# Performance work log

Measured on AMD Instinct MI355X. Metric: run time of the kernel, lower is better.

Reference implementation:

```python
import jax, jax.numpy as jnp
import numpy as np


def setup_inputs() -> dict:
    key = jax.random.key(0)
    x = jax.random.normal(key, (128, 256, 32, 32), dtype=jnp.float32)
    return {"x": x, "iter_num": 5}


def reference(x, iter_num):
    # x: (B, C, H, W)
    B, C, H, W = x.shape
    N = H * W
    xr = x.reshape(B, C, N)
    # Covariance pooling: X @ I_hat @ X^T == (1/N) * Xc @ Xc^T  (I_hat = I/N - J/N^2)
    xc = xr - xr.mean(axis=2, keepdims=True)
    cov = jnp.einsum('bcn,bdn->bcd', xc, xc) / N  # (B, C, C)

    # Newton-Schulz iterative matrix square root
    I = jnp.eye(C, dtype=x.dtype)
    I3 = 3.0 * I
    trace = jnp.trace(cov, axis1=1, axis2=2)[:, None, None]  # norm_A = tr(cov)
    A = cov / trace
    ZY = 0.5 * (I3 - A)
    Y = A @ ZY
    Z = ZY
    for _ in range(1, iter_num - 1):
        ZY = 0.5 * (I3 - Z @ Y)
        Y = Y @ ZY
        Z = ZY @ Z
    YZY = 0.5 * (Y @ (I3 - Z @ Y))
    sqrtm = YZY * jnp.sqrt(trace)  # (B, C, C)

    # Upper-triangular vectorization (row-major, including diagonal)
    r, c = np.triu_indices(C)
    idx = jnp.asarray(r * C + c)
    return sqrtm.reshape(B, C * C)[:, idx]  # (B, C*(C+1)//2)
```

## Files before the change

### kernel.cpp

```cpp
#include <hip/hip_runtime.h>
#include <hip/hip_fp16.h>


typedef _Float16 half8 __attribute__((ext_vector_type(8)));
typedef _Float16 half4 __attribute__((ext_vector_type(4)));
typedef float f32x4 __attribute__((ext_vector_type(4)));

#define OUTPB 32896

__device__ __forceinline__ void gl_lds16(const void* g, void* l) {
  __builtin_amdgcn_global_load_lds(
      (const __attribute__((address_space(1))) void*)g,
      (__attribute__((address_space(3))) void*)l, 16, 0, 0);
}

#define VMB(N) asm volatile("s_waitcnt vmcnt(" #N ")\n\ts_barrier" ::: "memory")
#define LKB()  asm volatile("s_waitcnt lgkmcnt(0)\n\ts_barrier" ::: "memory")

__device__ __forceinline__ void tile_pq(int t, int& p, int& q) {
  p = (t > 3) + (t > 6) + (t > 8);
  int base = p * 4 - (p * (p - 1)) / 2;
  q = p + (t - base);
}

__device__ __forceinline__ half8 cvt8(float4 a, float4 b) {
  half8 h;
  h[0] = (_Float16)a.x; h[1] = (_Float16)a.y; h[2] = (_Float16)a.z; h[3] = (_Float16)a.w;
  h[4] = (_Float16)b.x; h[5] = (_Float16)b.y; h[6] = (_Float16)b.z; h[7] = (_Float16)b.w;
  return h;
}

__device__ __forceinline__ void mfma64(const _Float16* lA, const _Float16* lB,
                                       f32x4 (&acc)[2][2], int wr, int wc,
                                       int lr, int lk) {
#pragma unroll
  for (int ks = 0; ks < 2; ++ks) {
    half8 af[2], bf[2];
#pragma unroll
    for (int m = 0; m < 2; ++m) {
      int row = wr * 32 + m * 16 + lr;
      int kc = (ks * 4 + lk) ^ (row & 7);
      af[m] = *(const half8*)&lA[row * 64 + kc * 8];
    }
#pragma unroll
    for (int n = 0; n < 2; ++n) {
      int row = wc * 32 + n * 16 + lr;
      int kc = (ks * 4 + lk) ^ (row & 7);
      bf[n] = *(const half8*)&lB[row * 64 + kc * 8];
    }
    __builtin_amdgcn_s_setprio(1);
#pragma unroll
    for (int m = 0; m < 2; ++m)
#pragma unroll
      for (int n = 0; n < 2; ++n)
        acc[m][n] = __builtin_amdgcn_mfma_f32_16x16x32_f16(af[m], bf[n], acc[m][n], 0, 0, 0);
    __builtin_amdgcn_s_setprio(0);
  }
}

template <typename F>
__device__ __forceinline__ void store_sym(F f, _Float16* D, size_t boff, int p, int q,
    bool mirror, _Float16* ldsT, f32x4 (&acc)[2][2],
    int wr, int wc, int lr, int lk, int tid) {
#pragma unroll
  for (int m = 0; m < 2; ++m)
#pragma unroll
    for (int n = 0; n < 2; ++n) {
      int il0 = wr * 32 + m * 16 + lk * 4;
      int jl = wc * 32 + n * 16 + lr;
      half4 v4;
#pragma unroll
      for (int r = 0; r < 4; ++r) {
        _Float16 v = f(acc[m][n][r], p * 64 + il0 + r, q * 64 + jl);
        v4[r] = v;
        if (mirror) ldsT[(il0 + r) * 64 + (jl ^ (((il0 + r) & 7) << 3))] = v;
      }
      *(half4*)&D[boff + (size_t)(q * 64 + jl) * 256 + p * 64 + il0] = v4;
    }
  if (mirror) {
    __syncthreads();
#pragma unroll
    for (int pp = 0; pp < 2; ++pp) {
      int u = pp * 256 + tid;
      int im = u >> 3, cu = u & 7;
      half8 v8 = *(const half8*)&ldsT[im * 64 + ((cu ^ (im & 7)) << 3)];
      *(half8*)&D[boff + (size_t)(p * 64 + im) * 256 + q * 64 + cu * 8] = v8;
    }
  }
}

__global__ __launch_bounds__(256, 2) void k_cov(const float* __restrict__ x,
                                                _Float16* __restrict__ covh,
                                                float* __restrict__ trPart) {
  __shared__ float lds_f[16384];
  __shared__ float sred[4];

  const int lin = blockIdx.x + 10 * blockIdx.y;
  const int cid = (lin & 7) * 160 + (lin >> 3);
  const int b = cid / 10, t = cid - 10 * b;
  int p, q; tile_pq(t, p, q);
  const bool diag = (p == q);
  const int tid = threadIdx.x, w = tid >> 6, lane = tid & 63;
  const int wr = w >> 1, wc = w & 1, lr = lane & 15, lk = lane >> 4;

  const float* Ab = x + ((size_t)b * 256 + p * 64) * 1024;
  const float* Bb = x + ((size_t)b * 256 + q * 64) * 1024;

  f32x4 acc[2][2] = {};
  f32x4 rsA[2] = {}, rsB[2] = {};
  half8 ones;
#pragma unroll
  for (int i = 0; i < 8; ++i) ones[i] = (_Float16)1.0f;

  auto stageF = [&](const float* panel, int buf, int baseF, int kk) {
#pragma unroll
    for (int i = 0; i < 4; ++i) {
      int s = (w * 4 + i) * 64 + lane;
      int row = s >> 4, cst = s & 15;
      int kc = cst ^ (row & 15);
      gl_lds16(panel + (size_t)row * 1024 + kk * 64 + kc * 4,
               &lds_f[baseF + buf * 4096 + (w * 4 + i) * 256]);
    }
  };

  auto step = [&](const float* lA, const float* lB) {
#pragma unroll
    for (int ks = 0; ks < 2; ++ks) {
      half8 af[2], bf[2];
#pragma unroll
      for (int m = 0; m < 2; ++m) {
        int row = wr * 32 + m * 16 + lr;
        int msk = row & 15, c0 = ks * 8 + lk * 2;
        float4 f0 = *(const float4*)&lA[row * 64 + (c0 ^ msk) * 4];
        float4 f1 = *(const float4*)&lA[row * 64 + ((c0 + 1) ^ msk) * 4];
        af[m] = cvt8(f0, f1);
      }
#pragma unroll
      for (int n = 0; n < 2; ++n) {
        int row = wc * 32 + n * 16 + lr;
        int msk = row & 15, c0 = ks * 8 + lk * 2;
        float4 f0 = *(const float4*)&lB[row * 64 + (c0 ^ msk) * 4];
        float4 f1 = *(const float4*)&lB[row * 64 + ((c0 + 1) ^ msk) * 4];
        bf[n] = cvt8(f0, f1);
      }
      __builtin_amdgcn_s_setprio(1);
#pragma unroll
      for (int m = 0; m < 2; ++m)
        rsA[m] = __builtin_amdgcn_mfma_f32_16x16x32_f16(af[m], ones, rsA[m], 0, 0, 0);
#pragma unroll
      for (int n = 0; n < 2; ++n)
        rsB[n] = __builtin_amdgcn_mfma_f32_16x16x32_f16(ones, bf[n], rsB[n], 0, 0, 0);
#pragma unroll
      for (int m = 0; m < 2; ++m)
#pragma unroll
        for (int n = 0; n < 2; ++n)
          acc[m][n] = __builtin_amdgcn_mfma_f32_16x16x32_f16(af[m], bf[n], acc[m][n], 0, 0, 0);
      __builtin_amdgcn_s_setprio(0);
    }
  };

  stageF(Ab, 0, 0, 0);
  if (!diag) stageF(Bb, 0, 8192, 0);
#pragma unroll 1
  for (int kk = 0; kk < 16; ++kk) {
    int cur = kk & 1;
    if (kk < 15) {
      stageF(Ab, cur ^ 1, 0, kk + 1);
      if (!diag) stageF(Bb, cur ^ 1, 8192, kk + 1);
      if (diag) { VMB(4); } else { VMB(8); }
    } else {
      VMB(0);
    }
    step(&lds_f[cur * 4096], diag ? &lds_f[cur * 4096] : &lds_f[8192 + cur * 4096]);
    LKB();
  }

  const float inv = 1.f / 1024.f;
  if (diag) {
    float tp = 0.f;
#pragma unroll
    for (int m = 0; m < 2; ++m)
#pragma unroll
      for (int n = 0; n < 2; ++n)
#pragma unroll
        for (int r = 0; r < 4; ++r) {
          int il = wr * 32 + m * 16 + lk * 4 + r, jl = wc * 32 + n * 16 + lr;
          if (il == jl) tp += (acc[m][n][r] - rsA[m][r] * rsB[n][0] * inv) * inv;
        }
#pragma unroll
    for (int o = 32; o; o >>= 1) tp += __shfl_down(tp, o);
    if (lane == 0) sred[w] = tp;
    __syncthreads();
    if (tid == 0) trPart[b * 4 + p] = sred[0] + sred[1] + sred[2] + sred[3];
  }

  _Float16* ldsh = (_Float16*)lds_f;
  const size_t boff = (size_t)b * 65536;
#pragma unroll
  for (int m = 0; m < 2; ++m)
#pragma unroll
    for (int n = 0; n < 2; ++n) {
      int il0 = wr * 32 + m * 16 + lk * 4;
      int jl = wc * 32 + n * 16 + lr;
      half4 v4;
#pragma unroll
      for (int r = 0; r < 4; ++r) {
        float cv = (acc[m][n][r] - rsA[m][r] * rsB[n][0] * inv) * inv;
        v4[r] = (_Float16)cv;
        if (!diag) ldsh[(il0 + r) * 64 + (jl ^ (((il0 + r) & 7) << 3))] = v4[r];
      }
      *(half4*)&covh[boff + (size_t)(q * 64 + jl) * 256 + p * 64 + il0] = v4;
    }
  if (!diag) {
    __syncthreads();
#pragma unroll
    for (int pp = 0; pp < 2; ++pp) {
      int u = pp * 256 + tid;
      int im = u >> 3, cu = u & 7;
      half8 v8 = *(const half8*)&ldsh[im * 64 + ((cu ^ (im & 7)) << 3)];
      *(half8*)&covh[boff + (size_t)(p * 64 + im) * 256 + q * 64 + cu * 8] = v8;
    }
  }
}

enum { EPI_S2 = 0, EPI_ZY = 1, EPI_OUT = 2 };

struct GP {
  const _Float16 *A0, *B0;
  _Float16 *D0, *D1;
  const _Float16* covh;
  const float* trP;
  float* outF;
};

template <int EPI>
__global__ __launch_bounds__(256, 4) void k_gemm(GP g) {
  __shared__ _Float16 lds[(EPI == EPI_S2) ? 8192 : 16384];

  const int lin = blockIdx.x + 10 * blockIdx.y;
  const int cid = (lin & 7) * 160 + (lin >> 3);
  const int b = cid / 10, t = cid - 10 * b;
  int p, q; tile_pq(t, p, q);
  const bool diag = (p == q);
  constexpr bool share = (EPI == EPI_S2);
  const int tid = threadIdx.x, w = tid >> 6, lane = tid & 63;
  const int wr = w >> 1, wc = w & 1, lr = lane & 15, lk = lane >> 4;

  const size_t boff = (size_t)b * 65536;
  const _Float16* Ap = g.A0 + boff + (size_t)p * 64 * 256;
  const _Float16* Bp = (share ? g.A0 : g.B0) + boff + (size_t)q * 64 * 256;

  f32x4 acc[2][2] = {};

  auto stageH = [&](const _Float16* panel, int buf, int base, int kk) {
#pragma unroll
    for (int i = 0; i < 2; ++i) {
      int s = (w * 2 + i) * 64 + lane;
      int row = s >> 3, cst = s & 7;
      int kc = cst ^ (row & 7);
      gl_lds16(panel + (size_t)row * 256 + kk * 64 + kc * 8,
               &lds[base + buf * 4096 + (w * 2 + i) * 512]);
    }
  };

  stageH(Ap, 0, 0, 0);
  if (!share) stageH(Bp, 0, 8192, 0);
#pragma unroll 1
  for (int kk = 0; kk < 4; ++kk) {
    int cur = kk & 1;
    if (kk < 3) {
      stageH(Ap, cur ^ 1, 0, kk + 1);
      if (!share) stageH(Bp, cur ^ 1, 8192, kk + 1);
      if (share) { VMB(2); } else { VMB(4); }
    } else {
      VMB(0);
    }
    mfma64(&lds[cur * 4096], share ? &lds[cur * 4096] : &lds[8192 + cur * 4096],
           acc, wr, wc, lr, lk);
    LKB();
  }

  if constexpr (EPI == EPI_ZY) {
    store_sym([&](float a, int i, int j) {
                return (_Float16)((i == j ? 1.5f : 0.f) - 0.5f * a);
              }, g.D0, boff, p, q, !diag, lds, acc, wr, wc, lr, lk, tid);
  } else if constexpr (EPI == EPI_S2) {
    float tv = g.trP[b * 4] + g.trP[b * 4 + 1] + g.trP[b * 4 + 2] + g.trP[b * 4 + 3];
    float it1 = 1.f / tv;
    _Float16* TY = lds;
    _Float16* TZ = lds + 4096;
#pragma unroll
    for (int m = 0; m < 2; ++m)
#pragma unroll
      for (int n = 0; n < 2; ++n) {
        int il0 = wr * 32 + m * 16 + lk * 4;
        int jl = wc * 32 + n * 16 + lr;
        half4 c4 = *(const half4*)&g.covh[boff + (size_t)(q * 64 + jl) * 256 + p * 64 + il0];
        half4 y4, z4;
#pragma unroll
        for (int r = 0; r < 4; ++r) {
          int i = p * 64 + il0 + r, j = q * 64 + jl;
          float c = (float)c4[r];
          y4[r] = (_Float16)(1.5f * c * it1 - 0.5f * acc[m][n][r] * it1 * it1);
          z4[r] = (_Float16)((i == j ? 1.5f : 0.f) - 0.5f * c * it1);
          if (!diag) {
            int sp = (il0 + r) * 64 + (jl ^ (((il0 + r) & 7) << 3));
            TY[sp] = y4[r]; TZ[sp] = z4[r];
          }
        }
        *(half4*)&g.D0[boff + (size_t)(q * 64 + jl) * 256 + p * 64 + il0] = y4;
        *(half4*)&g.D1[boff + (size_t)(q * 64 + jl) * 256 + p * 64 + il0] = z4;
      }
    if (!diag) {
      __syncthreads();
#pragma unroll
      for (int pp = 0; pp < 2; ++pp) {
        int u = pp * 256 + tid;
        int im = u >> 3, cu = u & 7;
        half8 vy = *(const half8*)&TY[im * 64 + ((cu ^ (im & 7)) << 3)];
        half8 vz = *(const half8*)&TZ[im * 64 + ((cu ^ (im & 7)) << 3)];
        *(half8*)&g.D0[boff + (size_t)(p * 64 + im) * 256 + q * 64 + cu * 8] = vy;
        *(half8*)&g.D1[boff + (size_t)(p * 64 + im) * 256 + q * 64 + cu * 8] = vz;
      }
    }
  } else {
    float tv = g.trP[b * 4] + g.trP[b * 4 + 1] + g.trP[b * 4 + 2] + g.trP[b * 4 + 3];
    float st = sqrtf(tv);
#pragma unroll
    for (int m = 0; m < 2; ++m)
#pragma unroll
      for (int n = 0; n < 2; ++n)
#pragma unroll
        for (int r = 0; r < 4; ++r) {
          int i = p * 64 + wr * 32 + m * 16 + lk * 4 + r;
          int j = q * 64 + wc * 32 + n * 16 + lr;
          if (i <= j) {
            int idx = j + i * 256 - (i * (i + 1)) / 2;
            g.outF[(size_t)b * OUTPB + idx] = acc[m][n][r] * st;
          }
        }
  }
}

struct YZP {
  const _Float16 *Y, *Z, *W;
  _Float16 *Yn, *Zn;
};

__global__ __launch_bounds__(256, 3) void k_yzm(YZP g) {
  __shared__ _Float16 lds[24576];

  const int lin = blockIdx.x + 10 * blockIdx.y;
  const int cid = (lin & 7) * 160 + (lin >> 3);
  const int b = cid / 10, t = cid - 10 * b;
  int p, q; tile_pq(t, p, q);
  const bool diag = (p == q);
  const int tid = threadIdx.x, w = tid >> 6, lane = tid & 63;
  const int wr = w >> 1, wc = w & 1, lr = lane & 15, lk = lane >> 4;

  const size_t boff = (size_t)b * 65536;
  const _Float16* Yp = g.Y + boff + (size_t)p * 64 * 256;
  const _Float16* Zp = g.Z + boff + (size_t)p * 64 * 256;
  const _Float16* Wp = g.W + boff + (size_t)q * 64 * 256;

  f32x4 accY[2][2] = {}, accZ[2][2] = {};

  auto stageH = [&](const _Float16* panel, int buf, int base, int kk) {
#pragma unroll
    for (int i = 0; i < 2; ++i) {
      int s = (w * 2 + i) * 64 + lane;
      int row = s >> 3, cst = s & 7;
      int kc = cst ^ (row & 7);
      gl_lds16(panel + (size_t)row * 256 + kk * 64 + kc * 8,
               &lds[base + buf * 4096 + (w * 2 + i) * 512]);
    }
  };

  auto step = [&](const _Float16* lY, const _Float16* lZ, const _Float16* lW) {
#pragma unroll
    for (int ks = 0; ks < 2; ++ks) {
      half8 yf[2], zf[2], wf[2];
#pragma unroll
      for (int m = 0; m < 2; ++m) {
        int row = wr * 32 + m * 16 + lr;
        int kc = (ks * 4 + lk) ^ (row & 7);
        yf[m] = *(const half8*)&lY[row * 64 + kc * 8];
        zf[m] = *(const half8*)&lZ[row * 64 + kc * 8];
      }
#pragma unroll
      for (int n = 0; n < 2; ++n) {
        int row = wc * 32 + n * 16 + lr;
        int kc = (ks * 4 + lk) ^ (row & 7);
        wf[n] = *(const half8*)&lW[row * 64 + kc * 8];
      }
      __builtin_amdgcn_s_setprio(1);
#pragma unroll
      for (int m = 0; m < 2; ++m)
#pragma unroll
        for (int n = 0; n < 2; ++n) {
          accY[m][n] = __builtin_amdgcn_mfma_f32_16x16x32_f16(yf[m], wf[n], accY[m][n], 0, 0, 0);
          accZ[m][n] = __builtin_amdgcn_mfma_f32_16x16x32_f16(zf[m], wf[n], accZ[m][n], 0, 0, 0);
        }
      __builtin_amdgcn_s_setprio(0);
    }
  };

  stageH(Yp, 0, 0, 0); stageH(Zp, 0, 8192, 0); stageH(Wp, 0, 16384, 0);
#pragma unroll 1
  for (int kk = 0; kk < 4; ++kk) {
    int cur = kk & 1;
    if (kk < 3) {
      stageH(Yp, cur ^ 1, 0, kk + 1);
      stageH(Zp, cur ^ 1, 8192, kk + 1);
      stageH(Wp, cur ^ 1, 16384, kk + 1);
      VMB(6);
    } else {
      VMB(0);
    }
    step(&lds[cur * 4096], &lds[8192 + cur * 4096], &lds[16384 + cur * 4096]);
    LKB();
  }

  _Float16* TY = lds;
  _Float16* TZ = lds + 4096;
#pragma unroll
  for (int m = 0; m < 2; ++m)
#pragma unroll
    for (int n = 0; n < 2; ++n) {
      int il0 = wr * 32 + m * 16 + lk * 4;
      int jl = wc * 32 + n * 16 + lr;
      half4 y4, z4;
#pragma unroll
      for (int r = 0; r < 4; ++r) {
        y4[r] = (_Float16)accY[m][n][r];
        z4[r] = (_Float16)accZ[m][n][r];
        if (!diag) {
          int sp = (il0 + r) * 64 + (jl ^ (((il0 + r) & 7) << 3));
          TY[sp] = y4[r]; TZ[sp] = z4[r];
        }
      }
      *(half4*)&g.Yn[boff + (size_t)(q * 64 + jl) * 256 + p * 64 + il0] = y4;
      *(half4*)&g.Zn[boff + (size_t)(q * 64 + jl) * 256 + p * 64 + il0] = z4;
    }
  if (!diag) {
    __syncthreads();
#pragma unroll
    for (int pp = 0; pp < 2; ++pp) {
      int u = pp * 256 + tid;
      int im = u >> 3, cu = u & 7;
      half8 vy = *(const half8*)&TY[im * 64 + ((cu ^ (im & 7)) << 3)];
      half8 vz = *(const half8*)&TZ[im * 64 + ((cu ^ (im & 7)) << 3)];
      *(half8*)&g.Yn[boff + (size_t)(p * 64 + im) * 256 + q * 64 + cu * 8] = vy;
      *(half8*)&g.Zn[boff + (size_t)(p * 64 + im) * 256 + q * 64 + cu * 8] = vz;
    }
  }
}

extern "C" void kernel_launch(void* const* d_in, const int* in_sizes, int n_in,
                              void* d_out, int out_size, void* d_ws, size_t ws_size,
                              hipStream_t stream) {
  const float* x = (const float*)d_in[0];
  float* outF = (float*)d_out;

  char* ws = (char*)d_ws;
  size_t off = 0;
  auto alloc = [&](size_t bytes) -> void* {
    void* pt = ws + off;
    off = (off + bytes + 255) & ~(size_t)255;
    return pt;
  };
  const size_t MATB = (size_t)128 * 65536 * sizeof(_Float16);
  _Float16* covh = (_Float16*)alloc(MATB);
  _Float16* Y0 = (_Float16*)alloc(MATB);
  _Float16* Z0 = (_Float16*)alloc(MATB);
  _Float16* Y1 = (_Float16*)alloc(MATB);
  _Float16* Z1 = (_Float16*)alloc(MATB);
  float* trP = (float*)alloc(512 * sizeof(float));

  dim3 g10(10, 128);

  k_cov<<<g10, 256, 0, stream>>>(x, covh, trP);

  {
    GP a{};
    a.A0 = covh; a.D0 = Y0; a.D1 = Z0;
    a.covh = covh; a.trP = trP;
    k_gemm<EPI_S2><<<g10, 256, 0, stream>>>(a);
  }

  _Float16 *Yc = Y0, *Zc = Z0, *Yn = Y1, *Zn = Z1;
  for (int itn = 0; itn < 3; ++itn) {
    GP a{};
    a.A0 = Zc; a.B0 = Yc; a.D0 = covh;
    k_gemm<EPI_ZY><<<g10, 256, 0, stream>>>(a);
    YZP r{};
    r.Y = Yc; r.Z = Zc; r.W = covh; r.Yn = Yn; r.Zn = Zn;
    k_yzm<<<g10, 256, 0, stream>>>(r);
    _Float16* t0 = Yc; Yc = Yn; Yn = t0;
    _Float16* t1 = Zc; Zc = Zn; Zn = t1;
  }
  {
    GP a{};
    a.A0 = Zc; a.B0 = Yc; a.D0 = covh;
    k_gemm<EPI_ZY><<<g10, 256, 0, stream>>>(a);
    GP o{};
    o.A0 = Yc; o.B0 = covh; o.trP = trP; o.outF = outF;
    k_gemm<EPI_OUT><<<g10, 256, 0, stream>>>(o);
  }
}
```

Measured before the change: 169.8 us.

## Split covariance into fp16 centering pass plus fp16 GEMM

Adds a k_center kernel that subtracts each row's mean and writes the centered input as fp16. The covariance GEMM then streams half-width data straight into LDS, which removes the in-loop fp32-to-fp16 conversion and the extra row-sum MFMAs. The workspace is reshaped so xc aliases Y0, k_gemm's S2 variant shares LDS only on diagonal tiles, and k_yzm's occupancy hint goes from 3 to 4. In exchange there is an extra kernel launch and a full write and re-read of a 64 MB fp16 intermediate.

```diff
diff --git a/kernel.cpp b/kernel.cpp
--- a/kernel.cpp
+++ b/kernel.cpp
@@ -21,13 +21,6 @@
   p = (t > 3) + (t > 6) + (t > 8);
   int base = p * 4 - (p * (p - 1)) / 2;
   q = p + (t - base);
-}
-
-__device__ __forceinline__ half8 cvt8(float4 a, float4 b) {
-  half8 h;
-  h[0] = (_Float16)a.x; h[1] = (_Float16)a.y; h[2] = (_Float16)a.z; h[3] = (_Float16)a.w;
-  h[4] = (_Float16)b.x; h[5] = (_Float16)b.y; h[6] = (_Float16)b.z; h[7] = (_Float16)b.w;
-  return h;
 }
 
 __device__ __forceinline__ void mfma64(const _Float16* lA, const _Float16* lB,
@@ -89,10 +82,40 @@
   }
 }
 
-__global__ __launch_bounds__(256, 2) void k_cov(const float* __restrict__ x,
-                                                _Float16* __restrict__ covh,
-                                                float* __restrict__ trPart) {
-  __shared__ float lds_f[16384];
+__global__ __launch_bounds__(256) void k_center(const float* __restrict__ x,
+                                                _Float16* __restrict__ xc) {
+  int gw = blockIdx.x * 4 + (threadIdx.x >> 6);
+  int lane = threadIdx.x & 63;
+#pragma unroll 1
+  for (int rr = 0; rr < 4; ++rr) {
+    int r = gw * 4 + rr;
+    const float4* rp = (const float4*)(x + (size_t)r * 1024);
+    float4 v0 = rp[2 * lane], v1 = rp[2 * lane + 1];
+    float4 v2 = rp[128 + 2 * lane], v3 = rp[128 + 2 * lane + 1];
+    float s = v0.x + v0.y + v0.z + v0.w + v1.x + v1.y + v1.z + v1.w +
+              v2.x + v2.y + v2.z + v2.w + v3.x + v3.y + v3.z + v3.w;
+#pragma unroll
+    for (int o = 1; o < 64; o <<= 1) s += __shfl_xor(s, o);
+    float mn = s * (1.f / 1024.f);
+    _Float16* orow = xc + (size_t)r * 1024;
+    half8 h;
+    h[0] = (_Float16)(v0.x - mn); h[1] = (_Float16)(v0.y - mn);
+    h[2] = (_Float16)(v0.z - mn); h[3] = (_Float16)(v0.w - mn);
+    h[4] = (_Float16)(v1.x - mn); h[5] = (_Float16)(v1.y - mn);
+    h[6] = (_Float16)(v1.z - mn); h[7] = (_Float16)(v1.w - mn);
+    *(half8*)&orow[lane * 8] = h;
+    h[0] = (_Float16)(v2.x - mn); h[1] = (_Float16)(v2.y - mn);
+    h[2] = (_Float16)(v2.z - mn); h[3] = (_Float16)(v2.w - mn);
+    h[4] = (_Float16)(v3.x - mn); h[5] = (_Float16)(v3.y - mn);
+    h[6] = (_Float16)(v3.z - mn); h[7] = (_Float16)(v3.w - mn);
+    *(half8*)&orow[512 + lane * 8] = h;
+  }
+}
+
+__global__ __launch_bounds__(256, 4) void k_covg(const _Float16* __restrict__ xc,
+                                                 _Float16* __restrict__ covh,
+                                                 float* __restrict__ trPart) {
+  __shared__ _Float16 lds[16384];
   __shared__ float sred[4];
 
   const int lin = blockIdx.x + 10 * blockIdx.y;
@@ -103,75 +126,40 @@
   const int tid = threadIdx.x, w = tid >> 6, lane = tid & 63;
   const int wr = w >> 1, wc = w & 1, lr = lane & 15, lk = lane >> 4;
 
-  const float* Ab = x + ((size_t)b * 256 + p * 64) * 1024;
-  const float* Bb = x + ((size_t)b * 256 + q * 64) * 1024;
+  const _Float16* Ap = xc + ((size_t)b * 256 + p * 64) * 1024;
+  const _Float16* Bp = xc + ((size_t)b * 256 + q * 64) * 1024;
 
   f32x4 acc[2][2] = {};
-  f32x4 rsA[2] = {}, rsB[2] = {};
-  half8 ones;
-#pragma unroll
-  for (int i = 0; i < 8; ++i) ones[i] = (_Float16)1.0f;
-
-  auto stageF = [&](const float* panel, int buf, int baseF, int kk) {
-#pragma unroll
-    for (int i = 0; i < 4; ++i) {
-      int s = (w * 4 + i) * 64 + lane;
-      int row = s >> 4, cst = s & 15;
-      int kc = cst ^ (row & 15);
-      gl_lds16(panel + (size_t)row * 1024 + kk * 64 + kc * 4,
-               &lds_f[baseF + buf * 4096 + (w * 4 + i) * 256]);
+
+  auto stageH = [&](const _Float16* panel, int buf, int base, int kk) {
+#pragma unroll
+    for (int i = 0; i < 2; ++i) {
+      int s = (w * 2 + i) * 64 + lane;
+      int row = s >> 3, cst = s & 7;
+      int kc = cst ^ (row & 7);
+      gl_lds16(panel + (size_t)row * 1024 + kk * 64 + kc * 8,
+               &lds[base + buf * 4096 + (w * 2 + i) * 512]);
     }
   };
 
-  auto step = [&](const float* lA, const float* lB) {
-#pragma unroll
-    for (int ks = 0; ks < 2; ++ks) {
-      half8 af[2], bf[2];
-#pragma unroll
-      for (int m = 0; m < 2; ++m) {
-        int row = wr * 32 + m * 16 + lr;
-        int msk = row & 15, c0 = ks * 8 + lk * 2;
-        float4 f0 = *(const float4*)&lA[row * 64 + (c0 ^ msk) * 4];
-        float4 f1 = *(const float4*)&lA[row * 64 + ((c0 + 1) ^ msk) * 4];
-        af[m] = cvt8(f0, f1);
-      }
-#pragma unroll
-      for (int n = 0; n < 2; ++n) {
-        int row = wc * 32 + n * 16 + lr;
-        int msk = row & 15, c0 = ks * 8 + lk * 2;
-        float4 f0 = *(const float4*)&lB[row * 64 + (c0 ^ msk) * 4];
-        float4 f1 = *(const float4*)&lB[row * 64 + ((c0 + 1) ^ msk) * 4];
-        bf[n] = cvt8(f0, f1);
-      }
-      __builtin_amdgcn_s_setprio(1);
-#pragma unroll
-      for (int m = 0; m < 2; ++m)
-        rsA[m] = __builtin_amdgcn_mfma_f32_16x16x32_f16(af[m], ones, rsA[m], 0, 0, 0);
-#pragma unroll
-      for (int n = 0; n < 2; ++n)
-        rsB[n] = __builtin_amdgcn_mfma_f32_16x16x32_f16(ones, bf[n], rsB[n], 0, 0, 0);
-#pragma unroll
-      for (int m = 0; m < 2; ++m)
-#pragma unroll
-        for (int n = 0; n < 2; ++n)
-          acc[m][n] = __builtin_amdgcn_mfma_f32_16x16x32_f16(af[m], bf[n], acc[m][n], 0, 0, 0);
-      __builtin_amdgcn_s_setprio(0);
-    }
-  };
-
-  stageF(Ab, 0, 0, 0);
-  if (!diag) stageF(Bb, 0, 8192, 0);
+  stageH(Ap, 0, 0, 0);
+  if (!diag) stageH(Bp, 0, 8192, 0);
 #pragma unroll 1
   for (int kk = 0; kk < 16; ++kk) {
     int cur = kk & 1;
     if (kk < 15) {
-      stageF(Ab, cur ^ 1, 0, kk + 1);
-      if (!diag) stageF(Bb, cur ^ 1, 8192, kk + 1);
-      if (diag) { VMB(4); } else { VMB(8); }
+      stageH(Ap, cur ^ 1, 0, kk + 1);
+      if (!diag) {
+        stageH(Bp, cur ^ 1, 8192, kk + 1);
+        VMB(4);
+      } else {
+        VMB(2);
+      }
     } else {
       VMB(0);
     }
-    step(&lds_f[cur * 4096], diag ? &lds_f[cur * 4096] : &lds_f[8192 + cur * 4096]);
+    mfma64(&lds[cur * 4096], diag ? &lds[cur * 4096] : &lds[8192 + cur * 4096],
+           acc, wr, wc, lr, lk);
     LKB();
   }
 
@@ -185,42 +173,18 @@
 #pragma unroll
         for (int r = 0; r < 4; ++r) {
           int il = wr * 32 + m * 16 + lk * 4 + r, jl = wc * 32 + n * 16 + lr;
-          if (il == jl) tp += (acc[m][n][r] - rsA[m][r] * rsB[n][0] * inv) * inv;
+          if (il == jl) tp += acc[m][n][r] * inv;
         }
 #pragma unroll
     for (int o = 32; o; o >>= 1) tp += __shfl_down(tp, o);
     if (lane == 0) sred[w] = tp;
     __syncthreads();
     if (tid == 0) trPart[b * 4 + p] = sred[0] + sred[1] + sred[2] + sred[3];
-  }
-
-  _Float16* ldsh = (_Float16*)lds_f;
-  const size_t boff = (size_t)b * 65536;
-#pragma unroll
-  for (int m = 0; m < 2; ++m)
-#pragma unroll
-    for (int n = 0; n < 2; ++n) {
-      int il0 = wr * 32 + m * 16 + lk * 4;
-      int jl = wc * 32 + n * 16 + lr;
-      half4 v4;
-#pragma unroll
-      for (int r = 0; r < 4; ++r) {
-        float cv = (acc[m][n][r] - rsA[m][r] * rsB[n][0] * inv) * inv;
-        v4[r] = (_Float16)cv;
-        if (!diag) ldsh[(il0 + r) * 64 + (jl ^ (((il0 + r) & 7) << 3))] = v4[r];
-      }
-      *(half4*)&covh[boff + (size_t)(q * 64 + jl) * 256 + p * 64 + il0] = v4;
-    }
-  if (!diag) {
     __syncthreads();
-#pragma unroll
-    for (int pp = 0; pp < 2; ++pp) {
-      int u = pp * 256 + tid;
-      int im = u >> 3, cu = u & 7;
-      half8 v8 = *(const half8*)&ldsh[im * 64 + ((cu ^ (im & 7)) << 3)];
-      *(half8*)&covh[boff + (size_t)(p * 64 + im) * 256 + q * 64 + cu * 8] = v8;
-    }
-  }
+  }
+
+  store_sym([&](float a, int i, int j) { return (_Float16)(a * inv); },
+            covh, (size_t)b * 65536, p, q, !diag, lds, acc, wr, wc, lr, lk, tid);
 }
 
 enum { EPI_S2 = 0, EPI_ZY = 1, EPI_OUT = 2 };
@@ -235,20 +199,20 @@
 
 template <int EPI>
 __global__ __launch_bounds__(256, 4) void k_gemm(GP g) {
-  __shared__ _Float16 lds[(EPI == EPI_S2) ? 8192 : 16384];
+  __shared__ _Float16 lds[16384];
 
   const int lin = blockIdx.x + 10 * blockIdx.y;
   const int cid = (lin & 7) * 160 + (lin >> 3);
   const int b = cid / 10, t = cid - 10 * b;
   int p, q; tile_pq(t, p, q);
   const bool diag = (p == q);
-  constexpr bool share = (EPI == EPI_S2);
+  const bool share = diag && (EPI == EPI_S2);
   const int tid = threadIdx.x, w = tid >> 6, lane = tid & 63;
   const int wr = w >> 1, wc = w & 1, lr = lane & 15, lk = lane >> 4;
 
   const size_t boff = (size_t)b * 65536;
   const _Float16* Ap = g.A0 + boff + (size_t)p * 64 * 256;
-  const _Float16* Bp = (share ? g.A0 : g.B0) + boff + (size_t)q * 64 * 256;
+  const _Float16* Bp = ((EPI == EPI_S2) ? g.A0 : g.B0) + boff + (size_t)q * 64 * 256;
 
   f32x4 acc[2][2] = {};
 
@@ -270,8 +234,12 @@
     int cur = kk & 1;
     if (kk < 3) {
       stageH(Ap, cur ^ 1, 0, kk + 1);
-      if (!share) stageH(Bp, cur ^ 1, 8192, kk + 1);
-      if (share) { VMB(2); } else { VMB(4); }
+      if (!share) {
+        stageH(Bp, cur ^ 1, 8192, kk + 1);
+        VMB(4);
+      } else {
+        VMB(2);
+      }
     } else {
       VMB(0);
     }
@@ -347,7 +315,7 @@
   _Float16 *Yn, *Zn;
 };
 
-__global__ __launch_bounds__(256, 3) void k_yzm(YZP g) {
+__global__ __launch_bounds__(256, 4) void k_yzm(YZP g) {
   __shared__ _Float16 lds[24576];
 
   const int lin = blockIdx.x + 10 * blockIdx.y;
@@ -463,23 +431,19 @@
   float* outF = (float*)d_out;
 
   char* ws = (char*)d_ws;
-  size_t off = 0;
-  auto alloc = [&](size_t bytes) -> void* {
-    void* pt = ws + off;
-    off = (off + bytes + 255) & ~(size_t)255;
-    return pt;
-  };
   const size_t MATB = (size_t)128 * 65536 * sizeof(_Float16);
-  _Float16* covh = (_Float16*)alloc(MATB);
-  _Float16* Y0 = (_Float16*)alloc(MATB);
-  _Float16* Z0 = (_Float16*)alloc(MATB);
-  _Float16* Y1 = (_Float16*)alloc(MATB);
-  _Float16* Z1 = (_Float16*)alloc(MATB);
-  float* trP = (float*)alloc(512 * sizeof(float));
+  _Float16* xc   = (_Float16*)ws;
+  _Float16* Y0   = (_Float16*)ws;
+  _Float16* Z0   = (_Float16*)(ws + MATB);
+  _Float16* Y1   = (_Float16*)(ws + 2 * MATB);
+  _Float16* Z1   = (_Float16*)(ws + 3 * MATB);
+  _Float16* covh = (_Float16*)(ws + 4 * MATB);
+  float* trP     = (float*)(ws + 5 * MATB);
 
   dim3 g10(10, 128);
 
-  k_cov<<<g10, 256, 0, stream>>>(x, covh, trP);
+  k_center<<<2048, 256, 0, stream>>>(x, xc);
+  k_covg<<<g10, 256, 0, stream>>>(xc, covh, trP);
 
   {
     GP a{};
```

New measurement: 179.4 us. 5.7% more time.

## Use 128x128 covariance tiles with register-staged fp16 conversion into LDS

Applied to the files above, without the earlier changes.

The covariance kernel moves from ten 64x64 upper-triangle tiles per batch to three 128x128 tiles. Each warp now computes a 64x64 sub-tile (4x4 MFMA fragments). Global fp32 loads are staged through registers and converted to fp16 once before being written to LDS, replacing the global_load_lds path that re-converted fp32 on every fragment read. This is meant to cut redundant reads of x and conversion work, but it raises register pressure, uses fewer blocks (384 instead of 1280), and adds plain __syncthreads pipelining. The S2 GEMM is adjusted to read the two-part trace and to stop sharing its LDS panel on off-diagonal tiles.

```diff
diff --git a/kernel.cpp b/kernel.cpp
--- a/kernel.cpp
+++ b/kernel.cpp
@@ -92,133 +92,138 @@
 __global__ __launch_bounds__(256, 2) void k_cov(const float* __restrict__ x,
                                                 _Float16* __restrict__ covh,
                                                 float* __restrict__ trPart) {
-  __shared__ float lds_f[16384];
+  __shared__ _Float16 lds[32768];
   __shared__ float sred[4];
 
-  const int lin = blockIdx.x + 10 * blockIdx.y;
-  const int cid = (lin & 7) * 160 + (lin >> 3);
-  const int b = cid / 10, t = cid - 10 * b;
-  int p, q; tile_pq(t, p, q);
-  const bool diag = (p == q);
+  const int lin = blockIdx.x + 3 * blockIdx.y;
+  const int cid = (lin & 7) * 48 + (lin >> 3);
+  const int b = cid / 3, t = cid - 3 * b;
+  const int p = (t == 1), q = (t != 0);
+  const bool diag = (t < 2);
   const int tid = threadIdx.x, w = tid >> 6, lane = tid & 63;
   const int wr = w >> 1, wc = w & 1, lr = lane & 15, lk = lane >> 4;
 
-  const float* Ab = x + ((size_t)b * 256 + p * 64) * 1024;
-  const float* Bb = x + ((size_t)b * 256 + q * 64) * 1024;
-
-  f32x4 acc[2][2] = {};
-  f32x4 rsA[2] = {}, rsB[2] = {};
+  const float* Ab = x + ((size_t)b * 256 + p * 128) * 1024;
+  const float* Bb = x + ((size_t)b * 256 + q * 128) * 1024;
+
+  float4 la[4][2], lb[4][2];
+  f32x4 acc[4][4] = {};
+  f32x4 rsA[4] = {}, rsB[4] = {};
   half8 ones;
 #pragma unroll
   for (int i = 0; i < 8; ++i) ones[i] = (_Float16)1.0f;
 
-  auto stageF = [&](const float* panel, int buf, int baseF, int kk) {
+  auto LOAD = [&](int kk) {
 #pragma unroll
     for (int i = 0; i < 4; ++i) {
-      int s = (w * 4 + i) * 64 + lane;
-      int row = s >> 4, cst = s & 15;
-      int kc = cst ^ (row & 15);
-      gl_lds16(panel + (size_t)row * 1024 + kk * 64 + kc * 4,
-               &lds_f[baseF + buf * 4096 + (w * 4 + i) * 256]);
+      int u = i * 256 + tid;
+      int row = u >> 3, c8 = u & 7;
+      int kc = c8 ^ (row & 7);
+      const float* sa = Ab + (size_t)row * 1024 + kk * 64 + kc * 8;
+      la[i][0] = *(const float4*)sa; la[i][1] = *(const float4*)(sa + 4);
+      if (!diag) {
+        const float* sb = Bb + (size_t)row * 1024 + kk * 64 + kc * 8;
+        lb[i][0] = *(const float4*)sb; lb[i][1] = *(const float4*)(sb + 4);
+      }
     }
   };
-
-  auto step = [&](const float* lA, const float* lB) {
+  auto WRITE = [&](int buf) {
+#pragma unroll
+    for (int i = 0; i < 4; ++i) {
+      int u = i * 256 + tid;
+      *(half8*)&lds[buf * 8192 + u * 8] = cvt8(la[i][0], la[i][1]);
+      if (!diag) *(half8*)&lds[16384 + buf * 8192 + u * 8] = cvt8(lb[i][0], lb[i][1]);
+    }
+  };
+  auto STEP = [&](const _Float16* lA, const _Float16* lB) {
 #pragma unroll
     for (int ks = 0; ks < 2; ++ks) {
-      half8 af[2], bf[2];
-#pragma unroll
-      for (int m = 0; m < 2; ++m) {
-        int row = wr * 32 + m * 16 + lr;
-        int msk = row & 15, c0 = ks * 8 + lk * 2;
-        float4 f0 = *(const float4*)&lA[row * 64 + (c0 ^ msk) * 4];
-        float4 f1 = *(const float4*)&lA[row * 64 + ((c0 + 1) ^ msk) * 4];
-        af[m] = cvt8(f0, f1);
-      }
-#pragma unroll
-      for (int n = 0; n < 2; ++n) {
-        int row = wc * 32 + n * 16 + lr;
-        int msk = row & 15, c0 = ks * 8 + lk * 2;
-        float4 f0 = *(const float4*)&lB[row * 64 + (c0 ^ msk) * 4];
-        float4 f1 = *(const float4*)&lB[row * 64 + ((c0 + 1) ^ msk) * 4];
-        bf[n] = cvt8(f0, f1);
+      half8 af[4], bf[4];
+#pragma unroll
+      for (int m = 0; m < 4; ++m) {
+        int row = wr * 64 + m * 16 + lr;
+        int kc = (ks * 4 + lk) ^ (row & 7);
+        af[m] = *(const half8*)&lA[row * 64 + kc * 8];
+      }
+#pragma unroll
+      for (int n = 0; n < 4; ++n) {
+        int row = wc * 64 + n * 16 + lr;
+        int kc = (ks * 4 + lk) ^ (row & 7);
+        bf[n] = *(const half8*)&lB[row * 64 + kc * 8];
       }
       __builtin_amdgcn_s_setprio(1);
 #pragma unroll
-      for (int m = 0; m < 2; ++m)
+      for (int m = 0; m < 4; ++m)
         rsA[m] = __builtin_amdgcn_mfma_f32_16x16x32_f16(af[m], ones, rsA[m], 0, 0, 0);
 #pragma unroll
-      for (int n = 0; n < 2; ++n)
+      for (int n = 0; n < 4; ++n)
         rsB[n] = __builtin_amdgcn_mfma_f32_16x16x32_f16(ones, bf[n], rsB[n], 0, 0, 0);
 #pragma unroll
-      for (int m = 0; m < 2; ++m)
-#pragma unroll
-        for (int n = 0; n < 2; ++n)
+      for (int m = 0; m < 4; ++m)
+#pragma unroll
+        for (int n = 0; n < 4; ++n)
           acc[m][n] = __builtin_amdgcn_mfma_f32_16x16x32_f16(af[m], bf[n], acc[m][n], 0, 0, 0);
       __builtin_amdgcn_s_setprio(0);
     }
   };
 
-  stageF(Ab, 0, 0, 0);
-  if (!diag) stageF(Bb, 0, 8192, 0);
+  LOAD(0); WRITE(0); LOAD(1);
+  __syncthreads();
 #pragma unroll 1
   for (int kk = 0; kk < 16; ++kk) {
     int cur = kk & 1;
+    STEP(&lds[cur * 8192], diag ? &lds[cur * 8192] : &lds[16384 + cur * 8192]);
     if (kk < 15) {
-      stageF(Ab, cur ^ 1, 0, kk + 1);
-      if (!diag) stageF(Bb, cur ^ 1, 8192, kk + 1);
-      if (diag) { VMB(4); } else { VMB(8); }
-    } else {
-      VMB(0);
-    }
-    step(&lds_f[cur * 4096], diag ? &lds_f[cur * 4096] : &lds_f[8192 + cur * 4096]);
-    LKB();
+      WRITE(cur ^ 1);
+      if (kk < 14) LOAD(kk + 2);
+    }
+    __syncthreads();
   }
 
   const float inv = 1.f / 1024.f;
   if (diag) {
     float tp = 0.f;
 #pragma unroll
-    for (int m = 0; m < 2; ++m)
-#pragma unroll
-      for (int n = 0; n < 2; ++n)
+    for (int m = 0; m < 4; ++m)
+#pragma unroll
+      for (int n = 0; n < 4; ++n)
 #pragma unroll
         for (int r = 0; r < 4; ++r) {
-          int il = wr * 32 + m * 16 + lk * 4 + r, jl = wc * 32 + n * 16 + lr;
+          int il = wr * 64 + m * 16 + lk * 4 + r, jl = wc * 64 + n * 16 + lr;
           if (il == jl) tp += (acc[m][n][r] - rsA[m][r] * rsB[n][0] * inv) * inv;
         }
 #pragma unroll
     for (int o = 32; o; o >>= 1) tp += __shfl_down(tp, o);
     if (lane == 0) sred[w] = tp;
     __syncthreads();
-    if (tid == 0) trPart[b * 4 + p] = sred[0] + sred[1] + sred[2] + sred[3];
-  }
-
-  _Float16* ldsh = (_Float16*)lds_f;
+    if (tid == 0) trPart[b * 2 + p] = sred[0] + sred[1] + sred[2] + sred[3];
+  }
+
   const size_t boff = (size_t)b * 65536;
 #pragma unroll
-  for (int m = 0; m < 2; ++m)
-#pragma unroll
-    for (int n = 0; n < 2; ++n) {
-      int il0 = wr * 32 + m * 16 + lk * 4;
-      int jl = wc * 32 + n * 16 + lr;
+  for (int m = 0; m < 4; ++m)
+#pragma unroll
+    for (int n = 0; n < 4; ++n) {
+      int il0 = wr * 64 + m * 16 + lk * 4;
+      int jl = wc * 64 + n * 16 + lr;
       half4 v4;
 #pragma unroll
       for (int r = 0; r < 4; ++r) {
+        int il = il0 + r;
         float cv = (acc[m][n][r] - rsA[m][r] * rsB[n][0] * inv) * inv;
         v4[r] = (_Float16)cv;
-        if (!diag) ldsh[(il0 + r) * 64 + (jl ^ (((il0 + r) & 7) << 3))] = v4[r];
-      }
-      *(half4*)&covh[boff + (size_t)(q * 64 + jl) * 256 + p * 64 + il0] = v4;
+        if (!diag) lds[il * 128 + (((jl >> 3) ^ (il & 7)) << 3) + (jl & 7)] = v4[r];
+      }
+      *(half4*)&covh[boff + (size_t)(q * 128 + jl) * 256 + p * 128 + il0] = v4;
     }
   if (!diag) {
     __syncthreads();
 #pragma unroll
-    for (int pp = 0; pp < 2; ++pp) {
+    for (int pp = 0; pp < 8; ++pp) {
       int u = pp * 256 + tid;
-      int im = u >> 3, cu = u & 7;
-      half8 v8 = *(const half8*)&ldsh[im * 64 + ((cu ^ (im & 7)) << 3)];
-      *(half8*)&covh[boff + (size_t)(p * 64 + im) * 256 + q * 64 + cu * 8] = v8;
+      int im = u >> 4, cu = u & 15;
+      half8 v8 = *(const half8*)&lds[im * 128 + ((cu ^ (im & 7)) << 3)];
+      *(half8*)&covh[boff + (size_t)(p * 128 + im) * 256 + q * 128 + cu * 8] = v8;
     }
   }
 }
@@ -235,20 +240,20 @@
 
 template <int EPI>
 __global__ __launch_bounds__(256, 4) void k_gemm(GP g) {
-  __shared__ _Float16 lds[(EPI == EPI_S2) ? 8192 : 16384];
+  __shared__ _Float16 lds[16384];
 
   const int lin = blockIdx.x + 10 * blockIdx.y;
   const int cid = (lin & 7) * 160 + (lin >> 3);
   const int b = cid / 10, t = cid - 10 * b;
   int p, q; tile_pq(t, p, q);
   const bool diag = (p == q);
-  constexpr bool share = (EPI == EPI_S2);
+  const bool share = diag && (EPI == EPI_S2);
   const int tid = threadIdx.x, w = tid >> 6, lane = tid & 63;
   const int wr = w >> 1, wc = w & 1, lr = lane & 15, lk = lane >> 4;
 
   const size_t boff = (size_t)b * 65536;
   const _Float16* Ap = g.A0 + boff + (size_t)p * 64 * 256;
-  const _Float16* Bp = (share ? g.A0 : g.B0) + boff + (size_t)q * 64 * 256;
+  const _Float16* Bp = ((EPI == EPI_S2) ? g.A0 : g.B0) + boff + (size_t)q * 64 * 256;
 
   f32x4 acc[2][2] = {};
 
@@ -270,8 +275,12 @@
     int cur = kk & 1;
     if (kk < 3) {
       stageH(Ap, cur ^ 1, 0, kk + 1);
-      if (!share) stageH(Bp, cur ^ 1, 8192, kk + 1);
-      if (share) { VMB(2); } else { VMB(4); }
+      if (!share) {
+        stageH(Bp, cur ^ 1, 8192, kk + 1);
+        VMB(4);
+      } else {
+        VMB(2);
+      }
     } else {
       VMB(0);
     }
@@ -285,7 +294,7 @@
                 return (_Float16)((i == j ? 1.5f : 0.f) - 0.5f * a);
               }, g.D0, boff, p, q, !diag, lds, acc, wr, wc, lr, lk, tid);
   } else if constexpr (EPI == EPI_S2) {
-    float tv = g.trP[b * 4] + g.trP[b * 4 + 1] + g.trP[b * 4 + 2] + g.trP[b * 4 + 3];
+    float tv = g.trP[b * 2] + g.trP[b * 2 + 1];
     float it1 = 1.f / tv;
     _Float16* TY = lds;
     _Float16* TZ = lds + 4096;
@@ -324,7 +333,7 @@
       }
     }
   } else {
-    float tv = g.trP[b * 4] + g.trP[b * 4 + 1] + g.trP[b * 4 + 2] + g.trP[b * 4 + 3];
+    float tv = g.trP[b * 2] + g.trP[b * 2 + 1];
     float st = sqrtf(tv);
 #pragma unroll
     for (int m = 0; m < 2; ++m)
@@ -463,23 +472,17 @@
   float* outF = (float*)d_out;
 
   char* ws = (char*)d_ws;
-  size_t off = 0;
-  auto alloc = [&](size_t bytes) -> void* {
-    void* pt = ws + off;
-    off = (off + bytes + 255) & ~(size_t)255;
-    return pt;
-  };
   const size_t MATB = (size_t)128 * 65536 * sizeof(_Float16);
-  _Float16* covh = (_Float16*)alloc(MATB);
-  _Float16* Y0 = (_Float16*)alloc(MATB);
-  _Float16* Z0 = (_Float16*)alloc(MATB);
-  _Float16* Y1 = (_Float16*)alloc(MATB);
-  _Float16* Z1 = (_Float16*)alloc(MATB);
-  float* trP = (float*)alloc(512 * sizeof(float));
-
-  dim3 g10(10, 128);
-
-  k_cov<<<g10, 256, 0, stream>>>(x, covh, trP);
+  _Float16* covh = (_Float16*)ws;
+  _Float16* Y0   = (_Float16*)(ws + MATB);
+  _Float16* Z0   = (_Float16*)(ws + 2 * MATB);
+  _Float16* Y1   = (_Float16*)(ws + 3 * MATB);
+  _Float16* Z1   = (_Float16*)(ws + 4 * MATB);
+  float* trP     = (float*)(ws + 5 * MATB);
+
+  dim3 g3(3, 128), g10(10, 128);
+
+  k_cov<<<g3, 256, 0, stream>>>(x, covh, trP);
 
   {
     GP a{};
```

Result: faster. 159.0 us (-6.3%).
